# Kernel optimization log

Hardware: AMD Instinct MI355X
Metric: run time of the kernel (lower is better)

The kernel has to match this reference:

```python
import jax, jax.numpy as jnp
import numpy as np

DIM = 1024
NUM_ATT = 8
NUM_HEADS = 16
HEAD_DIM = DIM // NUM_HEADS
ROPE_BASE = 10000.0
NEG_INF = -1e9


def _rope(x):
    # x: [B, H, L, hd]; torchtune-style interleaved RoPE applied along the sequence axis.
    B, H, L, hd = x.shape
    pos = jnp.arange(L, dtype=jnp.float32)
    inv_freq = 1.0 / (ROPE_BASE ** (jnp.arange(0, hd, 2, dtype=jnp.float32) / hd))
    ang = pos[:, None] * inv_freq[None, :]          # [L, hd/2]
    cos = jnp.cos(ang)[None, None]                  # [1,1,L,hd/2]
    sin = jnp.sin(ang)[None, None]
    xr = x.reshape(B, H, L, hd // 2, 2)
    x0, x1 = xr[..., 0], xr[..., 1]
    out = jnp.stack([x0 * cos - x1 * sin, x1 * cos + x0 * sin], axis=-1)
    return out.reshape(B, H, L, hd).astype(x.dtype)


def setup_inputs() -> dict:
    key = jax.random.key(0)
    ks = jax.random.split(key, 7)
    B, L = 32, 512
    x = jax.random.normal(ks[0], (B, L, DIM), dtype=jnp.float32)
    s = 0.02  # init scale for numerical sanity (init choice, not math)
    query_projs = jax.random.normal(ks[1], (NUM_ATT, DIM, DIM), dtype=jnp.float32) * s
    key_projs = jax.random.normal(ks[2], (NUM_ATT, DIM, DIM), dtype=jnp.float32) * s
    value_projs = jax.random.normal(ks[3], (NUM_ATT, DIM, DIM), dtype=jnp.float32) * s
    out_projs = jax.random.normal(ks[4], (NUM_ATT, DIM, DIM), dtype=jnp.float32) * s
    router_w = jax.random.normal(ks[5], (DIM, NUM_ATT), dtype=jnp.float32) * s
    router_b = jnp.zeros((NUM_ATT,), dtype=jnp.float32)
    return {"x": x, "query_projs": query_projs, "key_projs": key_projs,
            "value_projs": value_projs, "out_projs": out_projs,
            "router_w": router_w, "router_b": router_b}


def reference(x, query_projs, key_projs, value_projs, out_projs, router_w, router_b):
    B, L, D = x.shape
    H, hd = NUM_HEADS, HEAD_DIM
    scale = hd ** -0.5

    # top-1 routing on mean-pooled tokens
    logits = x.mean(axis=1) @ router_w + router_b       # [B, E]
    attn_probs = jax.nn.softmax(logits, axis=-1)
    routes = jnp.argmax(attn_probs, axis=-1)            # [B] int

    # per-batch weight gather (the memory-bound irregular access) + bmm
    qw = query_projs[routes]                             # [B, D, D]
    kw = key_projs[routes]
    vw = value_projs[routes]
    q = jnp.einsum('bld,bde->ble', x, qw)
    k = jnp.einsum('bld,bde->ble', x, kw)
    v = jnp.einsum('bld,bde->ble', x, vw)

    q = q.reshape(B, L, H, hd).transpose(0, 2, 1, 3)     # [B,H,L,hd]
    k = k.reshape(B, L, H, hd).transpose(0, 2, 1, 3)
    v = v.reshape(B, L, H, hd).transpose(0, 2, 1, 3)

    q = _rope(q)
    k = _rope(k)

    scores = jnp.einsum('bhld,bhmd->bhlm', q, k) * scale  # [B,H,L,L]
    causal = jnp.triu(jnp.ones((L, L), dtype=bool), k=1)  # True above diag = masked
    scores = jnp.where(causal[None, None], NEG_INF, scores)
    attn = jax.nn.softmax(scores, axis=-1)
    out = jnp.einsum('bhlm,bhmd->bhld', attn, v)          # [B,H,L,hd]
    out = out.transpose(0, 2, 1, 3).reshape(B, L, D)

    ow = out_projs[routes]                                # [B, D, D]
    out = jnp.einsum('bld,bde->ble', out, ow)
    return out, attn_probs
```

## Files before the change

kernel.cpp:

```cpp
#include <hip/hip_runtime.h>


typedef __attribute__((ext_vector_type(8))) short bf16x8;
typedef __attribute__((ext_vector_type(4))) float f32x4;

typedef const __attribute__((address_space(1))) unsigned short* gas_t;
typedef __attribute__((address_space(3))) unsigned short* las_t;

#define OFF_PART   (0ull)
#define OFF_ROUTES (2ull << 20)
#define OFF_XB     (3ull << 20)
#define OFF_WT     (40ull << 20)
#define OFF_QKV    (112ull << 20)

__device__ __forceinline__ unsigned short f2bf(float f){
  unsigned int u = __float_as_uint(f);
  u += 0x7fffu + ((u >> 16) & 1u);
  return (unsigned short)(u >> 16);
}


__global__ void meanpool_kernel(const float* __restrict__ x, float* __restrict__ part,
                                unsigned short* __restrict__ xb){
  const int b = blockIdx.x, lc = blockIdx.y, t = threadIdx.x;
  const size_t base = ((size_t)b*512 + lc*32)*1024;
  const float* xs = x + base;
  unsigned short* xo = xb + base;
  float a0=0.f, a1=0.f, a2=0.f, a3=0.f;
  for (int l = 0; l < 32; ++l){
    const float* row = xs + l*1024;
    unsigned short* orow = xo + l*1024;
    const float v0 = row[t], v1 = row[t+256], v2 = row[t+512], v3 = row[t+768];
    a0 += v0; a1 += v1; a2 += v2; a3 += v3;
    orow[t] = f2bf(v0); orow[t+256] = f2bf(v1); orow[t+512] = f2bf(v2); orow[t+768] = f2bf(v3);
  }
  float* o = part + ((size_t)b*16 + lc)*1024;
  o[t] = a0; o[t+256] = a1; o[t+512] = a2; o[t+768] = a3;
}

__global__ void router_kernel(const float* __restrict__ part,
                              const float* __restrict__ rw,
                              const float* __restrict__ rbias,
                              float* __restrict__ probs,
                              int* __restrict__ routes){
  const int b = blockIdx.x, t = threadIdx.x;
  __shared__ float xbar[1024];
  __shared__ float red[256*8];
  #pragma unroll
  for (int k = 0; k < 4; ++k){
    const int d = t + k*256;
    float s = 0.f;
    for (int lc = 0; lc < 16; ++lc) s += part[((size_t)b*16 + lc)*1024 + d];
    xbar[d] = s * (1.0f/512.0f);
  }
  __syncthreads();
  float p[8] = {0.f,0.f,0.f,0.f,0.f,0.f,0.f,0.f};
  #pragma unroll
  for (int k = 0; k < 4; ++k){
    const int d = t + k*256;
    const float xv = xbar[d];
    #pragma unroll
    for (int e = 0; e < 8; ++e) p[e] = fmaf(xv, rw[d*8 + e], p[e]);
  }
  #pragma unroll
  for (int e = 0; e < 8; ++e) red[t*8 + e] = p[e];
  __syncthreads();
  for (int s2 = 128; s2 > 0; s2 >>= 1){
    if (t < s2){
      #pragma unroll
      for (int e = 0; e < 8; ++e) red[t*8 + e] += red[(t + s2)*8 + e];
    }
    __syncthreads();
  }
  if (t == 0){
    float lg[8], mx = -3e38f; int am = 0;
    #pragma unroll
    for (int e = 0; e < 8; ++e){
      lg[e] = red[e] + rbias[e];
      if (lg[e] > mx){ mx = lg[e]; am = e; }
    }
    float sum = 0.f, ex[8];
    #pragma unroll
    for (int e = 0; e < 8; ++e){ ex[e] = __expf(lg[e] - mx); sum += ex[e]; }
    const float inv = 1.0f / sum;
    #pragma unroll
    for (int e = 0; e < 8; ++e) probs[b*8 + e] = ex[e] * inv;
    routes[b] = am;
  }
}


__global__ void wcast_kernel(const float* __restrict__ W, unsigned short* __restrict__ Wt){
  __shared__ float tile[32][33];
  const int mtx = blockIdx.z;
  const float* Wm = W + (size_t)mtx*1024*1024;
  unsigned short* Wo = Wt + (size_t)mtx*1024*1024;
  const int t = threadIdx.x;
  const int c = t & 31, r0 = t >> 5;
  const int gx = blockIdx.x*32, gy = blockIdx.y*32;
  #pragma unroll
  for (int k = 0; k < 4; ++k){
    const int r = r0 + k*8;
    tile[r][c] = Wm[(size_t)(gy + r)*1024 + gx + c];
  }
  __syncthreads();
  #pragma unroll
  for (int k = 0; k < 4; ++k){
    const int r = r0 + k*8;
    Wo[(size_t)(gx + r)*1024 + gy + c] = f2bf(tile[c][r]);
  }
}


template<int MODE>
__global__ __launch_bounds__(256, 2) void gemm_kernel(
    const unsigned short* __restrict__ A,
    const unsigned short* __restrict__ Wt,
    const int* __restrict__ routes,
    unsigned short* __restrict__ qkvout,
    float* __restrict__ outf)
{
  __shared__ __align__(16) unsigned short As[128*32];
  __shared__ __align__(16) unsigned short Bs[128*32];

  const int z = blockIdx.z;
  const int p = (MODE == 0) ? (z >> 5) : 0;
  const int b = (MODE == 0) ? (z & 31) : z;
  const int route = routes[b];
  const unsigned short* Ab = A + (size_t)b*512*1024;
  const unsigned short* Wb = Wt + (size_t)((MODE == 0) ? (p*8 + route) : route)*1024*1024;
  const int m0 = blockIdx.y * 128;
  const int n0 = blockIdx.x * 128;
  const int t = threadIdx.x;
  const int lane = t & 63;
  const int wave = t >> 6;
  const int wm = (wave >> 1) * 64;
  const int wn = (wave & 1) * 64;
  const int quad = lane >> 4;
  const int ln = lane & 15;

  f32x4 acc[4][4] = {};

  const int u0 = t, u1 = t + 256;
  const int r0s = u0 >> 2, c0s = (u0 & 3) ^ ((r0s >> 1) & 3);
  const int r1s = u1 >> 2, c1s = (u1 & 3) ^ ((r1s >> 1) & 3);
  const unsigned short* gA0 = Ab + (size_t)(m0 + r0s)*1024 + c0s*8;
  const unsigned short* gA1 = Ab + (size_t)(m0 + r1s)*1024 + c1s*8;
  const unsigned short* gB0 = Wb + (size_t)(n0 + r0s)*1024 + c0s*8;
  const unsigned short* gB1 = Wb + (size_t)(n0 + r1s)*1024 + c1s*8;
  las_t lA0 = (las_t)(As + u0*8), lA1 = (las_t)(As + u1*8);
  las_t lB0 = (las_t)(Bs + u0*8), lB1 = (las_t)(Bs + u1*8);

  const int swz = (quad ^ ((ln >> 1) & 3)) * 8;
  const unsigned short* fa[4];
  const unsigned short* fb[4];
  #pragma unroll
  for (int i = 0; i < 4; ++i){
    fa[i] = As + (wm + i*16 + ln)*32 + swz;
    fb[i] = Bs + (wn + i*16 + ln)*32 + swz;
  }

  for (int k0 = 0; k0 < 1024; k0 += 32){
    __syncthreads();
    __builtin_amdgcn_global_load_lds((gas_t)(gA0 + k0), lA0, 16, 0, 0);
    __builtin_amdgcn_global_load_lds((gas_t)(gA1 + k0), lA1, 16, 0, 0);
    __builtin_amdgcn_global_load_lds((gas_t)(gB0 + k0), lB0, 16, 0, 0);
    __builtin_amdgcn_global_load_lds((gas_t)(gB1 + k0), lB1, 16, 0, 0);
    __syncthreads();
    bf16x8 av[4], bv[4];
    #pragma unroll
    for (int i = 0; i < 4; ++i){
      av[i] = *(const bf16x8*)fa[i];
      bv[i] = *(const bf16x8*)fb[i];
    }
    #pragma unroll
    for (int i = 0; i < 4; ++i)
      #pragma unroll
      for (int j = 0; j < 4; ++j)
        acc[i][j] = __builtin_amdgcn_mfma_f32_16x16x32_bf16(av[i], bv[j], acc[i][j], 0, 0, 0);
  }

  if (MODE == 0){
    const size_t PSZ = (size_t)32*16*512*64;
    if (p < 2){
      #pragma unroll
      for (int j = 0; j < 4; ++j){
        const int e  = n0 + wn + j*16 + ln;
        const int h  = e >> 6;
        const int eh = e & 63;
        const float invf = exp2f(-0.41524101f * (float)(eh >> 1));
        unsigned short* outp = qkvout + ((((size_t)p*32 + b)*16 + h)*512)*64 + eh;
        #pragma unroll
        for (int i = 0; i < 4; ++i){
          #pragma unroll
          for (int r = 0; r < 4; ++r){
            const int l = m0 + wm + i*16 + quad*4 + r;
            const float own = acc[i][j][r];
            const float par = __shfl_xor(own, 1, 64);
            float sn, cs;
            __sincosf((float)l * invf, &sn, &cs);
            const float v = (e & 1) ? fmaf(own, cs, par*sn) : fmaf(own, cs, -par*sn);
            outp[(size_t)l*64] = f2bf(v);
          }
        }
      }
    } else {
      #pragma unroll
      for (int j = 0; j < 4; ++j){
        const int e  = n0 + wn + j*16 + ln;
        const int h  = e >> 6;
        const int eh = e & 63;
        unsigned short* outp = qkvout + 2*PSZ + (((size_t)b*16 + h)*64 + eh)*512;
        #pragma unroll
        for (int i = 0; i < 4; ++i){
          const int l0 = m0 + wm + i*16 + quad*4;
          ushort4 pk;
          pk.x = f2bf(acc[i][j][0]); pk.y = f2bf(acc[i][j][1]);
          pk.z = f2bf(acc[i][j][2]); pk.w = f2bf(acc[i][j][3]);
          *(ushort4*)(outp + l0) = pk;
        }
      }
    }
  } else {
    #pragma unroll
    for (int j = 0; j < 4; ++j){
      const int e = n0 + wn + j*16 + ln;
      #pragma unroll
      for (int i = 0; i < 4; ++i){
        #pragma unroll
        for (int r = 0; r < 4; ++r){
          const int l = m0 + wm + i*16 + quad*4 + r;
          outf[((size_t)b*512 + l)*1024 + e] = acc[i][j][r];
        }
      }
    }
  }
}


#define PSTR 72

__global__ __launch_bounds__(256, 3) void attn_kernel(
    const unsigned short* __restrict__ qkv,
    unsigned short* __restrict__ ctx)
{
  __shared__ __align__(16) unsigned short Ks[2][64*64];
  __shared__ __align__(16) unsigned short Vts[2][64*64];
  __shared__ __align__(16) unsigned short Ps[4][32*PSTR];

  const int qt = blockIdx.x, h = blockIdx.y, b = blockIdx.z;
  const size_t HO  = (((size_t)b)*16 + h)*512*64;
  const size_t PSZ = (size_t)32*16*512*64;
  const unsigned short* Qg  = qkv + HO;
  const unsigned short* Kg  = qkv + PSZ + HO;
  const unsigned short* Vtg = qkv + 2*PSZ + HO;

  const int t    = threadIdx.x;
  const int lane = t & 63;
  const int wave = t >> 6;
  const int quad = lane >> 4;
  const int ln   = lane & 15;

  const int u0 = t, u1 = t + 256;
  const int kr0 = u0 >> 3, kc0 = (u0 & 7) ^ (kr0 & 7);
  const int kr1 = u1 >> 3, kc1 = (u1 & 7) ^ (kr1 & 7);

  bf16x8 aq[2][2];
  #pragma unroll
  for (int rg = 0; rg < 2; ++rg){
    const int row = qt*128 + rg*64 + wave*16 + ln;
    #pragma unroll
    for (int ks = 0; ks < 2; ++ks)
      aq[rg][ks] = *(const bf16x8*)(Qg + (size_t)row*64 + ks*32 + quad*8);
  }

  const int ktEnd = 2*qt + 1;

  __builtin_amdgcn_global_load_lds((gas_t)(Kg  + kr0*64  + kc0*8), (las_t)(Ks[0]  + u0*8), 16,0,0);
  __builtin_amdgcn_global_load_lds((gas_t)(Kg  + kr1*64  + kc1*8), (las_t)(Ks[0]  + u1*8), 16,0,0);
  __builtin_amdgcn_global_load_lds((gas_t)(Vtg + kr0*512 + kc0*8), (las_t)(Vts[0] + u0*8), 16,0,0);
  __builtin_amdgcn_global_load_lds((gas_t)(Vtg + kr1*512 + kc1*8), (las_t)(Vts[0] + u1*8), 16,0,0);

  float m_r[2][4], l_r[2][4];
  #pragma unroll
  for (int rg = 0; rg < 2; ++rg)
    #pragma unroll
    for (int r = 0; r < 4; ++r){ m_r[rg][r] = -3e38f; l_r[rg][r] = 0.f; }
  f32x4 o[2][4] = {};

  const int swzl = ln & 7;
  unsigned short* Pw = Ps[wave];
  const int rowoff = wave*16 + quad*4;

  for (int kt = 0; kt <= ktEnd; ++kt){
    __syncthreads();
    if (kt < ktEnd){
      const unsigned short* Kn  = Kg + (kt+1)*4096;
      const int col = (kt+1)*64;
      unsigned short* kb = Ks[(kt+1)&1];
      unsigned short* vb = Vts[(kt+1)&1];
      __builtin_amdgcn_global_load_lds((gas_t)(Kn  + kr0*64 + kc0*8),        (las_t)(kb + u0*8), 16,0,0);
      __builtin_amdgcn_global_load_lds((gas_t)(Kn  + kr1*64 + kc1*8),        (las_t)(kb + u1*8), 16,0,0);
      __builtin_amdgcn_global_load_lds((gas_t)(Vtg + kr0*512 + col + kc0*8), (las_t)(vb + u0*8), 16,0,0);
      __builtin_amdgcn_global_load_lds((gas_t)(Vtg + kr1*512 + col + kc1*8), (las_t)(vb + u1*8), 16,0,0);
    }
    const unsigned short* ks_ = Ks[kt&1];
    const unsigned short* vt_ = Vts[kt&1];

    #pragma unroll
    for (int rg = 0; rg < 2; ++rg){
      if (rg == 0 && kt > 2*qt) continue;
      const bool diag = (kt == 2*qt + rg);

      f32x4 s[4] = {};
      #pragma unroll
      for (int ks2 = 0; ks2 < 2; ++ks2){
        #pragma unroll
        for (int kn = 0; kn < 4; ++kn){
          const bf16x8 bk = *(const bf16x8*)(ks_ + (kn*16+ln)*64 + (((quad + ks2*4) ^ swzl))*8);
          s[kn] = __builtin_amdgcn_mfma_f32_16x16x32_bf16(aq[rg][ks2], bk, s[kn], 0, 0, 0);
        }
      }

      float p[4][4], lm[4] = {-3e38f,-3e38f,-3e38f,-3e38f};
      #pragma unroll
      for (int kn = 0; kn < 4; ++kn){
        const int col = kn*16 + ln;
        #pragma unroll
        for (int r = 0; r < 4; ++r){
          float v = s[kn][r] * 0.125f;
          if (diag && col > rowoff + r) v = -1e9f;
          p[kn][r] = v;
          lm[r] = fmaxf(lm[r], v);
        }
      }
      #pragma unroll
      for (int off = 1; off < 16; off <<= 1)
        #pragma unroll
        for (int r = 0; r < 4; ++r)
          lm[r] = fmaxf(lm[r], __shfl_xor(lm[r], off, 64));
      float alpha[4], rsum[4];
      #pragma unroll
      for (int r = 0; r < 4; ++r){
        const float mn = fmaxf(m_r[rg][r], lm[r]);
        alpha[r] = __expf(m_r[rg][r] - mn);
        m_r[rg][r] = mn;
      }
      #pragma unroll
      for (int kn = 0; kn < 4; ++kn)
        #pragma unroll
        for (int r = 0; r < 4; ++r)
          p[kn][r] = __expf(p[kn][r] - m_r[rg][r]);
      #pragma unroll
      for (int r = 0; r < 4; ++r)
        rsum[r] = (p[0][r] + p[1][r]) + (p[2][r] + p[3][r]);
      #pragma unroll
      for (int off = 1; off < 16; off <<= 1)
        #pragma unroll
        for (int r = 0; r < 4; ++r)
          rsum[r] += __shfl_xor(rsum[r], off, 64);
      #pragma unroll
      for (int r = 0; r < 4; ++r) l_r[rg][r] = l_r[rg][r]*alpha[r] + rsum[r];
      #pragma unroll
      for (int dn = 0; dn < 4; ++dn)
        #pragma unroll
        for (int r = 0; r < 4; ++r)
          o[rg][dn][r] *= alpha[r];

      #pragma unroll
      for (int kn = 0; kn < 4; ++kn)
        #pragma unroll
        for (int r = 0; r < 4; ++r)
          Pw[(rg*16 + quad*4 + r)*PSTR + kn*16 + ln] = f2bf(p[kn][r]);

      #pragma unroll
      for (int ks2 = 0; ks2 < 2; ++ks2){
        const bf16x8 ap = *(const bf16x8*)(Pw + (rg*16 + ln)*PSTR + quad*8 + ks2*32);
        #pragma unroll
        for (int dn = 0; dn < 4; ++dn){
          const bf16x8 bv = *(const bf16x8*)(vt_ + (dn*16+ln)*64 + (((quad + ks2*4) ^ swzl))*8);
          o[rg][dn] = __builtin_amdgcn_mfma_f32_16x16x32_bf16(ap, bv, o[rg][dn], 0, 0, 0);
        }
      }
    }
  }

  #pragma unroll
  for (int rg = 0; rg < 2; ++rg){
    #pragma unroll
    for (int r = 0; r < 4; ++r){
      const float inv = 1.0f / l_r[rg][r];
      const int row = qt*128 + rg*64 + wave*16 + quad*4 + r;
      unsigned short* op = ctx + ((size_t)b*512 + row)*1024 + h*64 + ln;
      #pragma unroll
      for (int dn = 0; dn < 4; ++dn)
        op[dn*16] = f2bf(o[rg][dn][r] * inv);
    }
  }
}


extern "C" void kernel_launch(void* const* d_in, const int* in_sizes, int n_in,
                              void* d_out, int out_size, void* d_ws, size_t ws_size,
                              hipStream_t stream) {
  const float* x     = (const float*)d_in[0];
  const float* qw    = (const float*)d_in[1];
  const float* kw    = (const float*)d_in[2];
  const float* vw    = (const float*)d_in[3];
  const float* ow    = (const float*)d_in[4];
  const float* rw    = (const float*)d_in[5];
  const float* rbias = (const float*)d_in[6];
  float* out = (float*)d_out;
  char* ws = (char*)d_ws;

  float* part            = (float*)(ws + OFF_PART);
  int* routes            = (int*)(ws + OFF_ROUTES);
  unsigned short* xb     = (unsigned short*)(ws + OFF_XB);
  unsigned short* wt     = (unsigned short*)(ws + OFF_WT);
  unsigned short* qkvbuf = (unsigned short*)(ws + OFF_QKV);
  unsigned short* ctx    = xb;
  float* probs = out + (size_t)32*512*1024;

  meanpool_kernel<<<dim3(32, 16), 256, 0, stream>>>(x, part, xb);
  router_kernel<<<32, 256, 0, stream>>>(part, rw, rbias, probs, routes);
  wcast_kernel<<<dim3(32, 32, 8), 256, 0, stream>>>(qw, wt);
  wcast_kernel<<<dim3(32, 32, 8), 256, 0, stream>>>(kw, wt + (size_t)8*1024*1024);
  wcast_kernel<<<dim3(32, 32, 8), 256, 0, stream>>>(vw, wt + (size_t)16*1024*1024);
  wcast_kernel<<<dim3(32, 32, 8), 256, 0, stream>>>(ow, wt + (size_t)24*1024*1024);
  gemm_kernel<0><<<dim3(8, 4, 96), 256, 0, stream>>>(xb, wt, routes, qkvbuf, nullptr);
  attn_kernel<<<dim3(4, 16, 32), 256, 0, stream>>>(qkvbuf, ctx);
  gemm_kernel<1><<<dim3(8, 4, 32), 256, 0, stream>>>(ctx, wt + (size_t)24*1024*1024, routes,
                                                     nullptr, out);
}
```

Measured before the change: 561.7 us.

## Double-buffer GEMM LDS staging, remap workgroups across XCDs, cheapen RoPE, prioritize MFMA

The GEMM now uses two LDS buffers: the next K-slice is fetched with global_load_lds while MFMAs run on the current one, so there is one barrier per iteration instead of two. Both the GEMM and attention kernels flatten their block index and remap it so that neighbouring tiles sharing a batch or head land on the same XCD, which should improve L2 reuse. The RoPE epilogue replaces one sincos per row with one per 4 rows plus an angle-addition recurrence. In attention, MFMA sections get raised wave priority through s_setprio. The costs are double the GEMM LDS use, which may limit occupancy, small accumulated rounding error in the rotation, and a remap that hard-codes the grid sizes.

```diff
diff --git a/kernel.cpp b/kernel.cpp
--- a/kernel.cpp
+++ b/kernel.cpp
@@ -120,17 +120,21 @@
     unsigned short* __restrict__ qkvout,
     float* __restrict__ outf)
 {
-  __shared__ __align__(16) unsigned short As[128*32];
-  __shared__ __align__(16) unsigned short Bs[128*32];
-
-  const int z = blockIdx.z;
-  const int p = (MODE == 0) ? (z >> 5) : 0;
-  const int b = (MODE == 0) ? (z & 31) : z;
+  __shared__ __align__(16) unsigned short As[2][128*32];
+  __shared__ __align__(16) unsigned short Bs[2][128*32];
+
+  int wg = blockIdx.x + (blockIdx.y << 3) + (blockIdx.z << 5);
+  wg = (wg & 7) * ((MODE == 0) ? 384 : 128) + (wg >> 3);
+  const int z   = wg >> 5;
+  const int rem = wg & 31;
+  const int m0  = (rem >> 3) * 128;
+  const int n0  = (rem & 7) * 128;
+  const int b = (MODE == 0) ? (z / 3) : z;
+  const int p = (MODE == 0) ? (z - b*3) : 0;
+
   const int route = routes[b];
   const unsigned short* Ab = A + (size_t)b*512*1024;
   const unsigned short* Wb = Wt + (size_t)((MODE == 0) ? (p*8 + route) : route)*1024*1024;
-  const int m0 = blockIdx.y * 128;
-  const int n0 = blockIdx.x * 128;
   const int t = threadIdx.x;
   const int lane = t & 63;
   const int wave = t >> 6;
@@ -148,30 +152,37 @@
   const unsigned short* gA1 = Ab + (size_t)(m0 + r1s)*1024 + c1s*8;
   const unsigned short* gB0 = Wb + (size_t)(n0 + r0s)*1024 + c0s*8;
   const unsigned short* gB1 = Wb + (size_t)(n0 + r1s)*1024 + c1s*8;
-  las_t lA0 = (las_t)(As + u0*8), lA1 = (las_t)(As + u1*8);
-  las_t lB0 = (las_t)(Bs + u0*8), lB1 = (las_t)(Bs + u1*8);
+  las_t lA0 = (las_t)(&As[0][0] + u0*8), lA1 = (las_t)(&As[0][0] + u1*8);
+  las_t lB0 = (las_t)(&Bs[0][0] + u0*8), lB1 = (las_t)(&Bs[0][0] + u1*8);
 
   const int swz = (quad ^ ((ln >> 1) & 3)) * 8;
-  const unsigned short* fa[4];
-  const unsigned short* fb[4];
+  int offA[4], offB[4];
   #pragma unroll
   for (int i = 0; i < 4; ++i){
-    fa[i] = As + (wm + i*16 + ln)*32 + swz;
-    fb[i] = Bs + (wn + i*16 + ln)*32 + swz;
-  }
-
+    offA[i] = (wm + i*16 + ln)*32 + swz;
+    offB[i] = (wn + i*16 + ln)*32 + swz;
+  }
+
+#define STAGE(buf, kk) do { \
+    const int boff_ = (buf)*4096; \
+    __builtin_amdgcn_global_load_lds((gas_t)(gA0 + (kk)), lA0 + boff_, 16, 0, 0); \
+    __builtin_amdgcn_global_load_lds((gas_t)(gA1 + (kk)), lA1 + boff_, 16, 0, 0); \
+    __builtin_amdgcn_global_load_lds((gas_t)(gB0 + (kk)), lB0 + boff_, 16, 0, 0); \
+    __builtin_amdgcn_global_load_lds((gas_t)(gB1 + (kk)), lB1 + boff_, 16, 0, 0); \
+  } while (0)
+
+  STAGE(0, 0);
   for (int k0 = 0; k0 < 1024; k0 += 32){
+    const int cur = (k0 >> 5) & 1;
     __syncthreads();
-    __builtin_amdgcn_global_load_lds((gas_t)(gA0 + k0), lA0, 16, 0, 0);
-    __builtin_amdgcn_global_load_lds((gas_t)(gA1 + k0), lA1, 16, 0, 0);
-    __builtin_amdgcn_global_load_lds((gas_t)(gB0 + k0), lB0, 16, 0, 0);
-    __builtin_amdgcn_global_load_lds((gas_t)(gB1 + k0), lB1, 16, 0, 0);
-    __syncthreads();
+    if (k0 + 32 < 1024) STAGE(cur ^ 1, k0 + 32);
+    const unsigned short* Al = &As[cur][0];
+    const unsigned short* Bl = &Bs[cur][0];
     bf16x8 av[4], bv[4];
     #pragma unroll
     for (int i = 0; i < 4; ++i){
-      av[i] = *(const bf16x8*)fa[i];
-      bv[i] = *(const bf16x8*)fb[i];
+      av[i] = *(const bf16x8*)(Al + offA[i]);
+      bv[i] = *(const bf16x8*)(Bl + offB[i]);
     }
     #pragma unroll
     for (int i = 0; i < 4; ++i)
@@ -179,6 +190,7 @@
       for (int j = 0; j < 4; ++j)
         acc[i][j] = __builtin_amdgcn_mfma_f32_16x16x32_bf16(av[i], bv[j], acc[i][j], 0, 0, 0);
   }
+#undef STAGE
 
   if (MODE == 0){
     const size_t PSZ = (size_t)32*16*512*64;
@@ -189,18 +201,23 @@
         const int h  = e >> 6;
         const int eh = e & 63;
         const float invf = exp2f(-0.41524101f * (float)(eh >> 1));
+        float s1, c1; __sincosf(invf, &s1, &c1);
         unsigned short* outp = qkvout + ((((size_t)p*32 + b)*16 + h)*512)*64 + eh;
+        const int l0 = m0 + wm + quad*4;
         #pragma unroll
         for (int i = 0; i < 4; ++i){
+          float sn, cs;
+          __sincosf((float)(l0 + i*16) * invf, &sn, &cs);
           #pragma unroll
           for (int r = 0; r < 4; ++r){
-            const int l = m0 + wm + i*16 + quad*4 + r;
+            const int l = l0 + i*16 + r;
             const float own = acc[i][j][r];
             const float par = __shfl_xor(own, 1, 64);
-            float sn, cs;
-            __sincosf((float)l * invf, &sn, &cs);
             const float v = (e & 1) ? fmaf(own, cs, par*sn) : fmaf(own, cs, -par*sn);
             outp[(size_t)l*64] = f2bf(v);
+            const float nc = cs*c1 - sn*s1;
+            const float ns = sn*c1 + cs*s1;
+            cs = nc; sn = ns;
           }
         }
       }
@@ -248,7 +265,12 @@
   __shared__ __align__(16) unsigned short Vts[2][64*64];
   __shared__ __align__(16) unsigned short Ps[4][32*PSTR];
 
-  const int qt = blockIdx.x, h = blockIdx.y, b = blockIdx.z;
+  int wg = blockIdx.x + (blockIdx.y << 2) + (blockIdx.z << 6);
+  wg = (wg & 7) * 256 + (wg >> 3);
+  const int b  = wg >> 6;
+  const int h  = (wg >> 2) & 15;
+  const int qt = wg & 3;
+
   const size_t HO  = (((size_t)b)*16 + h)*512*64;
   const size_t PSZ = (size_t)32*16*512*64;
   const unsigned short* Qg  = qkv + HO;
@@ -313,6 +335,7 @@
       const bool diag = (kt == 2*qt + rg);
 
       f32x4 s[4] = {};
+      __builtin_amdgcn_s_setprio(1);
       #pragma unroll
       for (int ks2 = 0; ks2 < 2; ++ks2){
         #pragma unroll
@@ -321,6 +344,7 @@
           s[kn] = __builtin_amdgcn_mfma_f32_16x16x32_bf16(aq[rg][ks2], bk, s[kn], 0, 0, 0);
         }
       }
+      __builtin_amdgcn_s_setprio(0);
 
       float p[4][4], lm[4] = {-3e38f,-3e38f,-3e38f,-3e38f};
       #pragma unroll
@@ -373,6 +397,7 @@
         for (int r = 0; r < 4; ++r)
           Pw[(rg*16 + quad*4 + r)*PSTR + kn*16 + ln] = f2bf(p[kn][r]);
 
+      __builtin_amdgcn_s_setprio(1);
       #pragma unroll
       for (int ks2 = 0; ks2 < 2; ++ks2){
         const bf16x8 ap = *(const bf16x8*)(Pw + (rg*16 + ln)*PSTR + quad*8 + ks2*32);
@@ -382,6 +407,7 @@
           o[rg][dn] = __builtin_amdgcn_mfma_f32_16x16x32_bf16(ap, bv, o[rg][dn], 0, 0, 0);
         }
       }
+      __builtin_amdgcn_s_setprio(0);
     }
   }
 
```

Result: faster. 516.1 us (-8.1%).
